# Kernel tuning notes

Hardware: AMD Instinct MI355X
Metric: run time of the kernel (lower is better)

## Reference

```python
import math
import jax, jax.numpy as jnp
import numpy as np

B, N = 8, 2048
IN_DIM = COND_DIM = ATTN_DIM = OUT_DIM = 128
NUM_HEADS = 4
DH = ATTN_DIM // NUM_HEADS  # 32


def setup_inputs() -> dict:
    key = jax.random.key(0)
    ks = jax.random.split(key, 10)
    s_in = 1.0 / math.sqrt(IN_DIM)
    s_cd = 1.0 / math.sqrt(COND_DIM)
    return {
        "x": jax.random.normal(ks[0], (B, N, IN_DIM), jnp.float32),
        "cond": jax.random.normal(ks[1], (B, N, COND_DIM), jnp.float32),
        "flags": jnp.ones((B, N, 1), jnp.float32),
        "attention_mask": jax.random.normal(ks[2], (B, N, N), jnp.float32),
        # Linear params (stored [in, out]; torch Linear is x @ W.T + b)
        "Wq": jax.random.uniform(ks[3], (IN_DIM, ATTN_DIM), jnp.float32, -s_in, s_in),
        "bq": jax.random.uniform(ks[4], (ATTN_DIM,), jnp.float32, -s_in, s_in),
        "Wk": jax.random.uniform(ks[5], (COND_DIM, ATTN_DIM), jnp.float32, -s_cd, s_cd),
        "bk": jax.random.uniform(ks[6], (ATTN_DIM,), jnp.float32, -s_cd, s_cd),
        "Wv": jax.random.uniform(ks[7], (COND_DIM, OUT_DIM), jnp.float32, -s_cd, s_cd),
        "bv": jax.random.uniform(ks[8], (OUT_DIM,), jnp.float32, -s_cd, s_cd),
    }


def reference(x, cond, flags, attention_mask, Wq, bq, Wk, bk, Wv, bv):
    # flags is accepted but unused, matching the original forward.
    b, n, _ = x.shape
    Q = (x @ Wq + bq).reshape(b, n, NUM_HEADS, DH)     # channel-split heads
    K = (cond @ Wk + bk).reshape(b, n, NUM_HEADS, DH)
    V = cond @ Wv + bv                                 # [B, N, OUT_DIM]
    # per-head scores, scaled by sqrt(out_dim) as in the original
    S = jnp.einsum("bnhd,bmhd->hbnm", Q, K) / math.sqrt(OUT_DIM)
    A = jnp.tanh(attention_mask[None] + S)             # tanh activation, not softmax
    A = A.mean(axis=0)                                 # head-mean -> [B, N, N]
    return jnp.einsum("bnm,bmd->bnd", A, V)
```

## Files before the change

### kernel.cpp

```cpp
#include <hip/hip_runtime.h>
#include <hip/hip_bf16.h>

typedef __attribute__((ext_vector_type(4))) float f32x4;
typedef __attribute__((ext_vector_type(8))) short bf16x8;

#define MFMA16(A, B, C) __builtin_amdgcn_mfma_f32_16x16x32_bf16(A, B, C, 0, 0, 0)

#define C2 2.8853900817779268f
#define QS (2.8853900817779268f / 11.313708498984761f)

__device__ __forceinline__ unsigned cvtpk_bf16(float lo, float hi) {
    unsigned r;
    asm("v_cvt_pk_bf16_f32 %0, %1, %2" : "=v"(r) : "v"(lo), "v"(hi));
    return r;
}

__device__ __forceinline__ bf16x8 pack8(float4 a, float4 b) {
    union { unsigned u[4]; bf16x8 v; } u;
    u.u[0] = cvtpk_bf16(a.x, a.y);
    u.u[1] = cvtpk_bf16(a.z, a.w);
    u.u[2] = cvtpk_bf16(b.x, b.y);
    u.u[3] = cvtpk_bf16(b.z, b.w);
    return u.v;
}

__device__ __forceinline__ void gload_lds16(const void* g, void* l) {
    __builtin_amdgcn_global_load_lds(
        (const __attribute__((address_space(1))) unsigned int*)g,
        (__attribute__((address_space(3))) unsigned int*)l, 16, 0, 0);
}

__global__ void prep_weights(const float* __restrict__ Wq, const float* __restrict__ bq,
                             const float* __restrict__ Wk, const float* __restrict__ bk,
                             const float* __restrict__ Wv, const float* __restrict__ bv,
                             __hip_bfloat16* __restrict__ Wqt, __hip_bfloat16* __restrict__ Wkt,
                             __hip_bfloat16* __restrict__ Wvt, float* __restrict__ bias) {
    int i = blockIdx.x * 256 + threadIdx.x;
    int k = i >> 7, o = i & 127;
    Wqt[o * 128 + k] = __float2bfloat16(Wq[i] * QS);
    Wkt[o * 128 + k] = __float2bfloat16(Wk[i]);
    Wvt[o * 128 + k] = __float2bfloat16(Wv[i] * 0.25f);
    if (i < 128) {
        bias[i]       = bq[i] * QS;
        bias[128 + i] = bk[i];
        bias[256 + i] = bv[i] * 0.25f;
    }
}

__global__ __launch_bounds__(256) void proj_qkv(
        const float* __restrict__ x, const float* __restrict__ cond,
        const __hip_bfloat16* __restrict__ Wqt, const __hip_bfloat16* __restrict__ Wkt,
        const __hip_bfloat16* __restrict__ Wvt, const float* __restrict__ bias,
        __hip_bfloat16* __restrict__ Qo, __hip_bfloat16* __restrict__ Ko,
        __hip_bfloat16* __restrict__ Vt) {
    const int lane = threadIdx.x & 63, wv = threadIdx.x >> 6;
    const int l15 = lane & 15, g = lane >> 4;
    const int row0 = blockIdx.x * 64 + wv * 16;

    f32x4 qa[8], ka[8], va[8];
#pragma unroll
    for (int ot = 0; ot < 8; ++ot) {
        float b0 = bias[16 * ot + l15];
        float b1 = bias[128 + 16 * ot + l15];
        float b2 = bias[256 + 16 * ot + l15];
        qa[ot] = (f32x4){b0, b0, b0, b0};
        ka[ot] = (f32x4){b1, b1, b1, b1};
        va[ot] = (f32x4){b2, b2, b2, b2};
    }

    const float* xp = x    + (size_t)(row0 + l15) * 128 + 8 * g;
    const float* cp = cond + (size_t)(row0 + l15) * 128 + 8 * g;
#pragma unroll
    for (int kk = 0; kk < 4; ++kk) {
        float4 x0 = *(const float4*)(xp + 32 * kk);
        float4 x1 = *(const float4*)(xp + 32 * kk + 4);
        float4 c0 = *(const float4*)(cp + 32 * kk);
        float4 c1 = *(const float4*)(cp + 32 * kk + 4);
        bf16x8 xa = pack8(x0, x1);
        bf16x8 ca = pack8(c0, c1);
#pragma unroll
        for (int ot = 0; ot < 8; ++ot) {
            const int wo = (16 * ot + l15) * 128 + 32 * kk + 8 * g;
            qa[ot] = MFMA16(xa, *(const bf16x8*)(Wqt + wo), qa[ot]);
            ka[ot] = MFMA16(ca, *(const bf16x8*)(Wkt + wo), ka[ot]);
            va[ot] = MFMA16(ca, *(const bf16x8*)(Wvt + wo), va[ot]);
        }
    }

#pragma unroll
    for (int ot = 0; ot < 8; ++ot)
#pragma unroll
        for (int r = 0; r < 4; ++r) {
            size_t idx = (size_t)(row0 + 4 * g + r) * 128 + 16 * ot + l15;
            Qo[idx] = __float2bfloat16(qa[ot][r]);
            Ko[idx] = __float2bfloat16(ka[ot][r]);
        }
    const int bb = row0 >> 11, nn = (row0 & 2047) + 4 * g;
#pragma unroll
    for (int ot = 0; ot < 8; ++ot) {
        uint2 pr;
        pr.x = cvtpk_bf16(va[ot][0], va[ot][1]);
        pr.y = cvtpk_bf16(va[ot][2], va[ot][3]);
        *(uint2*)((unsigned short*)Vt + ((size_t)bb * 128 + 16 * ot + l15) * 2048 + nn) = pr;
    }
}

__global__ __launch_bounds__(512, 4) void attn_main(
        const __hip_bfloat16* __restrict__ Q, const __hip_bfloat16* __restrict__ K,
        const __hip_bfloat16* __restrict__ Vt, const float* __restrict__ mask,
        float* __restrict__ out) {
    __shared__ __align__(16) char Kl[2][16384];
    __shared__ __align__(16) char Vl[2][16384];
    __shared__ __align__(16) char Al[64 * 144];

    const int lane = threadIdx.x & 63, w = threadIdx.x >> 6;
    const int l15 = lane & 15, g = lane >> 4;
    const int qw = w & 3, mw = w >> 2, dw = mw;
    const int b  = blockIdx.x & 7;
    const int r2 = blockIdx.x >> 3;
    const int qt = r2 & 31;
    const int mh = r2 >> 5;
    const int n0 = qt * 64;
    const int mh0 = mh * 1024;

    const __hip_bfloat16* Qb = Q + ((size_t)b * 2048 + n0 + qw * 16) * 128;
    const char* Kg = (const char*)(K + (size_t)b * 2048 * 128);
    const char* Vg = (const char*)(Vt + (size_t)b * 128 * 2048);
    const float* mrow = mask + ((size_t)b * 2048 + n0 + qw * 16 + l15) * 2048
                        + mh0 + mw * 32 + 4 * g;

    bf16x8 qf[4];
#pragma unroll
    for (int h = 0; h < 4; ++h)
        qf[h] = *(const bf16x8*)(Qb + l15 * 128 + 32 * h + 8 * g);

    f32x4 oacc[4];
#pragma unroll
    for (int dtl = 0; dtl < 4; ++dtl) oacc[dtl] = (f32x4){0.f, 0.f, 0.f, 0.f};
    const f32x4 zero = (f32x4){0.f, 0.f, 0.f, 0.f};

    auto STAGE = [&](int m0g, int bi) {
#pragma unroll
        for (int i = 0; i < 2; ++i) {
            const int t = w * 2 + i;
            const int o = t * 1024 + lane * 16;
            const int kr = o >> 8, kc = o & 255;
            gload_lds16(Kg + (size_t)(m0g + kr) * 256 + (kc ^ ((kr & 7) << 4)),
                        &Kl[bi][t * 1024]);
            const int vr = o >> 7, vc = o & 127;
            gload_lds16(Vg + (size_t)vr * 4096 + (size_t)m0g * 2 + (vc ^ ((vr & 7) << 4)),
                        &Vl[bi][t * 1024]);
        }
    };

    STAGE(mh0, 0);
    f32x4 mkc0 = *(const f32x4*)(mrow);
    f32x4 mkc1 = *(const f32x4*)(mrow + 16);
    asm volatile("s_waitcnt vmcnt(0)" ::: "memory");
    __builtin_amdgcn_s_barrier();

#pragma unroll 2
    for (int c = 0; c < 16; ++c) {
        const int bi = c & 1;
        const int m0g = mh0 + c * 64;
        if (c < 15) STAGE(m0g + 64, bi ^ 1);
        f32x4 mkn0, mkn1;
        if (c < 15) {
            mkn0 = *(const f32x4*)(mrow + (c + 1) * 64);
            mkn1 = *(const f32x4*)(mrow + (c + 1) * 64 + 16);
        }

#pragma unroll
        for (int st = 0; st < 2; ++st) {
            const int mr = mw * 32 + st * 16 + l15;
            const char* kb = &Kl[bi][mr * 256];
            const int sw = (mr & 7) << 4;
            f32x4 s0 = MFMA16(*(const bf16x8*)(kb + ((g * 16) ^ sw)),       qf[0], zero);
            f32x4 s1 = MFMA16(*(const bf16x8*)(kb + ((64 + g * 16) ^ sw)),  qf[1], zero);
            f32x4 s2 = MFMA16(*(const bf16x8*)(kb + ((128 + g * 16) ^ sw)), qf[2], zero);
            f32x4 s3 = MFMA16(*(const bf16x8*)(kb + ((192 + g * 16) ^ sw)), qf[3], zero);
            const f32x4 mk = st ? mkc1 : mkc0;
            float acd[4];
#pragma unroll
            for (int r = 0; r < 4; ++r) {
                float t0 = 1.f + __builtin_amdgcn_exp2f(fmaf(mk[r], C2, s0[r]));
                float t1 = 1.f + __builtin_amdgcn_exp2f(fmaf(mk[r], C2, s1[r]));
                float t2 = 1.f + __builtin_amdgcn_exp2f(fmaf(mk[r], C2, s2[r]));
                float t3 = 1.f + __builtin_amdgcn_exp2f(fmaf(mk[r], C2, s3[r]));
                float p  = t0 * t1, q = t2 * t3;
                float nn = fmaf(t0 + t1, q, (t2 + t3) * p);
                float rs = nn * __builtin_amdgcn_rcpf(p * q);
                acd[r] = fmaf(-2.f, rs, 4.f);
            }
            uint2 pk;
            pk.x = cvtpk_bf16(acd[0], acd[1]);
            pk.y = cvtpk_bf16(acd[2], acd[3]);
            *(uint2*)(Al + (qw * 16 + l15) * 144 + (mw * 32 + st * 16 + 4 * g) * 2) = pk;
        }

        asm volatile("s_waitcnt lgkmcnt(0)" ::: "memory");
        __builtin_amdgcn_s_barrier();

#pragma unroll
        for (int ks = 0; ks < 2; ++ks) {
            bf16x8 af = *(const bf16x8*)(Al + (qw * 16 + l15) * 144 + (ks * 32 + 8 * g) * 2);
#pragma unroll
            for (int dtl = 0; dtl < 4; ++dtl) {
                const int dr = dw * 64 + dtl * 16 + l15;
                bf16x8 vf = *(const bf16x8*)(
                    &Vl[bi][dr * 128 + ((ks * 64 + g * 16) ^ ((dr & 7) << 4))]);
                oacc[dtl] = MFMA16(af, vf, oacc[dtl]);
            }
        }

        asm volatile("s_waitcnt vmcnt(0)" ::: "memory");
        __builtin_amdgcn_s_barrier();

        mkc0 = mkn0;
        mkc1 = mkn1;
    }

    float* ob = out + ((size_t)b * 2048 + n0 + qw * 16) * 128 + dw * 64;
#pragma unroll
    for (int dtl = 0; dtl < 4; ++dtl)
#pragma unroll
        for (int r = 0; r < 4; ++r)
            unsafeAtomicAdd(&ob[(size_t)(4 * g + r) * 128 + dtl * 16 + l15], oacc[dtl][r]);
}

extern "C" void kernel_launch(void* const* d_in, const int* in_sizes, int n_in,
                              void* d_out, int out_size, void* d_ws, size_t ws_size,
                              hipStream_t stream) {
    const float* x    = (const float*)d_in[0];
    const float* cond = (const float*)d_in[1];
    const float* mask = (const float*)d_in[3];
    const float* Wq = (const float*)d_in[4];
    const float* bq = (const float*)d_in[5];
    const float* Wk = (const float*)d_in[6];
    const float* bk = (const float*)d_in[7];
    const float* Wv = (const float*)d_in[8];
    const float* bv = (const float*)d_in[9];
    float* out = (float*)d_out;

    char* ws = (char*)d_ws;
    __hip_bfloat16* Qo  = (__hip_bfloat16*)(ws);
    __hip_bfloat16* Ko  = (__hip_bfloat16*)(ws + (4  << 20));
    __hip_bfloat16* Vt  = (__hip_bfloat16*)(ws + (8  << 20));
    __hip_bfloat16* Wqt = (__hip_bfloat16*)(ws + (12 << 20));
    __hip_bfloat16* Wkt = (__hip_bfloat16*)(ws + (12 << 20) + 32768);
    __hip_bfloat16* Wvt = (__hip_bfloat16*)(ws + (12 << 20) + 65536);
    float*          bias = (float*)(ws + (12 << 20) + 98304);

    hipMemsetAsync(d_out, 0, (size_t)out_size * sizeof(float), stream);

    prep_weights<<<64, 256, 0, stream>>>(Wq, bq, Wk, bk, Wv, bv, Wqt, Wkt, Wvt, bias);
    proj_qkv<<<256, 256, 0, stream>>>(x, cond, Wqt, Wkt, Wvt, bias, Qo, Ko, Vt);
    attn_main<<<512, 512, 0, stream>>>(Qo, Ko, Vt, mask, out);
}
```

Measured before the change: 86.72 us.

## Remap warps to 32x16 score tiles and 32x32 output tiles for fragment reuse

Changes the per-warp work split in the attention kernel. Each warp now computes two 16-row query groups against one 16-column key slice, so one set of K fragments is reused across both query groups. In the AV stage each V fragment feeds two MFMAs, which lowers LDS reads per MFMA. The cost is more registers for the doubled Q fragments and the 2x2 accumulators, which may reduce occupancy under the 512x4 launch bounds.

```diff
diff --git a/kernel.cpp b/kernel.cpp
--- a/kernel.cpp
+++ b/kernel.cpp
@@ -115,7 +115,9 @@
 
     const int lane = threadIdx.x & 63, w = threadIdx.x >> 6;
     const int l15 = lane & 15, g = lane >> 4;
-    const int qw = w & 3, mw = w >> 2, dw = mw;
+    const int qp = w & 1;
+    const int mt = w >> 1;
+    const int dp = w >> 1;
     const int b  = blockIdx.x & 7;
     const int r2 = blockIdx.x >> 3;
     const int qt = r2 & 31;
@@ -123,20 +125,25 @@
     const int n0 = qt * 64;
     const int mh0 = mh * 1024;
 
-    const __hip_bfloat16* Qb = Q + ((size_t)b * 2048 + n0 + qw * 16) * 128;
+    const __hip_bfloat16* Qb = Q + ((size_t)b * 2048 + n0 + qp * 32) * 128;
     const char* Kg = (const char*)(K + (size_t)b * 2048 * 128);
     const char* Vg = (const char*)(Vt + (size_t)b * 128 * 2048);
-    const float* mrow = mask + ((size_t)b * 2048 + n0 + qw * 16 + l15) * 2048
-                        + mh0 + mw * 32 + 4 * g;
-
-    bf16x8 qf[4];
-#pragma unroll
-    for (int h = 0; h < 4; ++h)
-        qf[h] = *(const bf16x8*)(Qb + l15 * 128 + 32 * h + 8 * g);
-
-    f32x4 oacc[4];
-#pragma unroll
-    for (int dtl = 0; dtl < 4; ++dtl) oacc[dtl] = (f32x4){0.f, 0.f, 0.f, 0.f};
+    const float* mrow0 = mask + ((size_t)b * 2048 + n0 + qp * 32 + l15) * 2048
+                         + mh0 + mt * 16 + 4 * g;
+    const float* mrow1 = mrow0 + (size_t)16 * 2048;
+
+    bf16x8 qf[2][4];
+#pragma unroll
+    for (int p = 0; p < 2; ++p)
+#pragma unroll
+        for (int h = 0; h < 4; ++h)
+            qf[p][h] = *(const bf16x8*)(Qb + (p * 16 + l15) * 128 + 32 * h + 8 * g);
+
+    f32x4 oacc[2][2];
+#pragma unroll
+    for (int i = 0; i < 2; ++i)
+#pragma unroll
+        for (int j = 0; j < 2; ++j) oacc[i][j] = (f32x4){0.f, 0.f, 0.f, 0.f};
     const f32x4 zero = (f32x4){0.f, 0.f, 0.f, 0.f};
 
     auto STAGE = [&](int m0g, int bi) {
@@ -154,8 +161,8 @@
     };
 
     STAGE(mh0, 0);
-    f32x4 mkc0 = *(const f32x4*)(mrow);
-    f32x4 mkc1 = *(const f32x4*)(mrow + 16);
+    f32x4 mkc0 = *(const f32x4*)(mrow0);
+    f32x4 mkc1 = *(const f32x4*)(mrow1);
     asm volatile("s_waitcnt vmcnt(0)" ::: "memory");
     __builtin_amdgcn_s_barrier();
 
@@ -166,36 +173,42 @@
         if (c < 15) STAGE(m0g + 64, bi ^ 1);
         f32x4 mkn0, mkn1;
         if (c < 15) {
-            mkn0 = *(const f32x4*)(mrow + (c + 1) * 64);
-            mkn1 = *(const f32x4*)(mrow + (c + 1) * 64 + 16);
-        }
-
-#pragma unroll
-        for (int st = 0; st < 2; ++st) {
-            const int mr = mw * 32 + st * 16 + l15;
+            mkn0 = *(const f32x4*)(mrow0 + (c + 1) * 64);
+            mkn1 = *(const f32x4*)(mrow1 + (c + 1) * 64);
+        }
+
+        {
+            const int mr = mt * 16 + l15;
             const char* kb = &Kl[bi][mr * 256];
             const int sw = (mr & 7) << 4;
-            f32x4 s0 = MFMA16(*(const bf16x8*)(kb + ((g * 16) ^ sw)),       qf[0], zero);
-            f32x4 s1 = MFMA16(*(const bf16x8*)(kb + ((64 + g * 16) ^ sw)),  qf[1], zero);
-            f32x4 s2 = MFMA16(*(const bf16x8*)(kb + ((128 + g * 16) ^ sw)), qf[2], zero);
-            f32x4 s3 = MFMA16(*(const bf16x8*)(kb + ((192 + g * 16) ^ sw)), qf[3], zero);
-            const f32x4 mk = st ? mkc1 : mkc0;
-            float acd[4];
-#pragma unroll
-            for (int r = 0; r < 4; ++r) {
-                float t0 = 1.f + __builtin_amdgcn_exp2f(fmaf(mk[r], C2, s0[r]));
-                float t1 = 1.f + __builtin_amdgcn_exp2f(fmaf(mk[r], C2, s1[r]));
-                float t2 = 1.f + __builtin_amdgcn_exp2f(fmaf(mk[r], C2, s2[r]));
-                float t3 = 1.f + __builtin_amdgcn_exp2f(fmaf(mk[r], C2, s3[r]));
-                float p  = t0 * t1, q = t2 * t3;
-                float nn = fmaf(t0 + t1, q, (t2 + t3) * p);
-                float rs = nn * __builtin_amdgcn_rcpf(p * q);
-                acd[r] = fmaf(-2.f, rs, 4.f);
+            bf16x8 kfr[4];
+#pragma unroll
+            for (int h = 0; h < 4; ++h)
+                kfr[h] = *(const bf16x8*)(kb + ((64 * h + 16 * g) ^ sw));
+#pragma unroll
+            for (int p = 0; p < 2; ++p) {
+                f32x4 s0 = MFMA16(kfr[0], qf[p][0], zero);
+                f32x4 s1 = MFMA16(kfr[1], qf[p][1], zero);
+                f32x4 s2 = MFMA16(kfr[2], qf[p][2], zero);
+                f32x4 s3 = MFMA16(kfr[3], qf[p][3], zero);
+                const f32x4 mk = p ? mkc1 : mkc0;
+                float acd[4];
+#pragma unroll
+                for (int r = 0; r < 4; ++r) {
+                    float t0 = 1.f + __builtin_amdgcn_exp2f(fmaf(mk[r], C2, s0[r]));
+                    float t1 = 1.f + __builtin_amdgcn_exp2f(fmaf(mk[r], C2, s1[r]));
+                    float t2 = 1.f + __builtin_amdgcn_exp2f(fmaf(mk[r], C2, s2[r]));
+                    float t3 = 1.f + __builtin_amdgcn_exp2f(fmaf(mk[r], C2, s3[r]));
+                    float pp = t0 * t1, qq = t2 * t3;
+                    float nn = fmaf(t0 + t1, qq, (t2 + t3) * pp);
+                    float rs = nn * __builtin_amdgcn_rcpf(pp * qq);
+                    acd[r] = fmaf(-2.f, rs, 4.f);
+                }
+                uint2 pk;
+                pk.x = cvtpk_bf16(acd[0], acd[1]);
+                pk.y = cvtpk_bf16(acd[2], acd[3]);
+                *(uint2*)(Al + (qp * 32 + p * 16 + l15) * 144 + (mt * 16 + 4 * g) * 2) = pk;
             }
-            uint2 pk;
-            pk.x = cvtpk_bf16(acd[0], acd[1]);
-            pk.y = cvtpk_bf16(acd[2], acd[3]);
-            *(uint2*)(Al + (qw * 16 + l15) * 144 + (mw * 32 + st * 16 + 4 * g) * 2) = pk;
         }
 
         asm volatile("s_waitcnt lgkmcnt(0)" ::: "memory");
@@ -203,13 +216,15 @@
 
 #pragma unroll
         for (int ks = 0; ks < 2; ++ks) {
-            bf16x8 af = *(const bf16x8*)(Al + (qw * 16 + l15) * 144 + (ks * 32 + 8 * g) * 2);
-#pragma unroll
-            for (int dtl = 0; dtl < 4; ++dtl) {
-                const int dr = dw * 64 + dtl * 16 + l15;
+            bf16x8 af0 = *(const bf16x8*)(Al + (qp * 32 + l15) * 144 + (ks * 32 + 8 * g) * 2);
+            bf16x8 af1 = *(const bf16x8*)(Al + (qp * 32 + 16 + l15) * 144 + (ks * 32 + 8 * g) * 2);
+#pragma unroll
+            for (int dt = 0; dt < 2; ++dt) {
+                const int dr = dp * 32 + dt * 16 + l15;
                 bf16x8 vf = *(const bf16x8*)(
                     &Vl[bi][dr * 128 + ((ks * 64 + g * 16) ^ ((dr & 7) << 4))]);
-                oacc[dtl] = MFMA16(af, vf, oacc[dtl]);
+                oacc[0][dt] = MFMA16(af0, vf, oacc[0][dt]);
+                oacc[1][dt] = MFMA16(af1, vf, oacc[1][dt]);
             }
         }
 
@@ -220,12 +235,15 @@
         mkc1 = mkn1;
     }
 
-    float* ob = out + ((size_t)b * 2048 + n0 + qw * 16) * 128 + dw * 64;
-#pragma unroll
-    for (int dtl = 0; dtl < 4; ++dtl)
-#pragma unroll
-        for (int r = 0; r < 4; ++r)
-            unsafeAtomicAdd(&ob[(size_t)(4 * g + r) * 128 + dtl * 16 + l15], oacc[dtl][r]);
+    float* ob = out + ((size_t)b * 2048 + n0 + qp * 32) * 128 + dp * 32;
+#pragma unroll
+    for (int qt2 = 0; qt2 < 2; ++qt2)
+#pragma unroll
+        for (int dt = 0; dt < 2; ++dt)
+#pragma unroll
+            for (int r = 0; r < 4; ++r)
+                unsafeAtomicAdd(&ob[(size_t)(qt2 * 16 + 4 * g + r) * 128 + dt * 16 + l15],
+                                oacc[qt2][dt][r]);
 }
 
 extern "C" void kernel_launch(void* const* d_in, const int* in_sizes, int n_in,
```

After: 87.36 us. Within noise of the previous version (+0.7%).
